# Kernel optimization log

Hardware: AMD Instinct MI355X
Metric: run time of the kernel (lower is better)

Reference implementation:

```python
import jax, jax.numpy as jnp
import numpy as np

N_NODES = 100000


def _add_self_loops(edge_index, n):
    loop = jnp.arange(n, dtype=edge_index.dtype)
    row = jnp.concatenate([edge_index[0], loop])
    col = jnp.concatenate([edge_index[1], loop])
    return row, col


def _gcn_conv(x, row, col, norm, W, b, n):
    # linear transform first (features shrink 512->16 before gather/scatter)
    h = x @ W                                  # [N, H]
    msg = h[row] * norm[:, None]               # [E+N, H] gather + scale
    out = jax.ops.segment_sum(msg, col, num_segments=n)  # scatter-add
    return out + b


def setup_inputs() -> dict:
    key = jax.random.key(0)
    ks = jax.random.split(key, 8)
    n, e, f, h = N_NODES, 3200000, 512, 16
    x = jax.random.normal(ks[0], (n, f), dtype=jnp.float32)
    edge_index = jax.random.randint(ks[1], (2, e), 0, n, dtype=jnp.int64)
    W1 = jax.random.normal(ks[2], (f, h), dtype=jnp.float32) / np.sqrt(f)
    b1 = jnp.zeros((h,), dtype=jnp.float32)
    W2 = jax.random.normal(ks[3], (h, h), dtype=jnp.float32) / np.sqrt(h)
    b2 = jnp.zeros((h,), dtype=jnp.float32)
    Wl = jax.random.normal(ks[4], (h, 1), dtype=jnp.float32) / np.sqrt(h)
    bl = jnp.zeros((1,), dtype=jnp.float32)
    return {"x": x, "edge_index": edge_index, "W1": W1, "b1": b1,
            "W2": W2, "b2": b2, "Wl": Wl, "bl": bl}


def reference(x, edge_index, W1, b1, W2, b2, Wl, bl):
    n = x.shape[0]
    row, col = _add_self_loops(edge_index, n)
    # symmetric GCN normalization: D^{-1/2} (A+I) D^{-1/2}
    deg = jax.ops.segment_sum(jnp.ones_like(col, dtype=x.dtype), col, num_segments=n)
    dinv = jnp.where(deg > 0, jax.lax.rsqrt(deg), 0.0)
    norm = dinv[row] * dinv[col]               # [E+N]

    out = jax.nn.relu(_gcn_conv(x, row, col, norm, W1, b1, n))
    out = jax.nn.relu(_gcn_conv(out, row, col, norm, W2, b2, n))
    return (out @ Wl + bl).reshape(-1)         # [N]
```

## Files before the change

kernel.cpp:

```cpp
#include <hip/hip_runtime.h>


#define NTHREADS 256

__global__ void hist_kernel(const int* __restrict__ col, int E, int n,
                            int* __restrict__ indeg) {
    int i = blockIdx.x * blockDim.x + threadIdx.x;
    int stride = gridDim.x * blockDim.x;
    for (; i < E; i += stride) {
        int c = col[i];
        if ((unsigned)c < (unsigned)n) atomicAdd(&indeg[c], 1);
    }
}

__global__ void dinv_kernel(const int* __restrict__ indeg,
                            float* __restrict__ dinv, int n) {
    int v = blockIdx.x * blockDim.x + threadIdx.x;
    if (v < n) dinv[v] = rsqrtf((float)(indeg[v] + 1));
}

__global__ void scan_block_sums(const int* __restrict__ indeg,
                                int* __restrict__ partial, int n) {
    __shared__ int s[NTHREADS];
    int t = threadIdx.x, i = blockIdx.x * NTHREADS + t;
    s[t] = (i < n) ? indeg[i] : 0;
    __syncthreads();
    for (int off = NTHREADS / 2; off > 0; off >>= 1) {
        if (t < off) s[t] += s[t + off];
        __syncthreads();
    }
    if (t == 0) partial[blockIdx.x] = s[0];
}

__global__ void scan_partials(int* __restrict__ partial, int nb,
                              int* __restrict__ rowptr, int n, int E) {
    __shared__ int s[512];
    int t = threadIdx.x;
    int v = (t < nb) ? partial[t] : 0;
    s[t] = v;
    __syncthreads();
    for (int off = 1; off < 512; off <<= 1) {
        int add = (t >= off) ? s[t - off] : 0;
        __syncthreads();
        s[t] += add;
        __syncthreads();
    }
    if (t < nb) partial[t] = s[t] - v;
    if (t == 0) rowptr[n] = E;
}

__global__ void scan_write(const int* __restrict__ indeg,
                           const int* __restrict__ partial,
                           int* __restrict__ rowptr, int n) {
    __shared__ int s[NTHREADS];
    int t = threadIdx.x, i = blockIdx.x * NTHREADS + t;
    int v = (i < n) ? indeg[i] : 0;
    s[t] = v;
    __syncthreads();
    for (int off = 1; off < NTHREADS; off <<= 1) {
        int add = (t >= off) ? s[t - off] : 0;
        __syncthreads();
        s[t] += add;
        __syncthreads();
    }
    if (i < n) rowptr[i] = partial[blockIdx.x] + s[t] - v;
}

__global__ void fill_kernel(const int* __restrict__ ei, int E, int n,
                            const int* __restrict__ rowptr,
                            int* __restrict__ cnt, int* __restrict__ adj) {
    int i = blockIdx.x * blockDim.x + threadIdx.x;
    int stride = gridDim.x * blockDim.x;
    for (; i < E; i += stride) {
        int r = ei[i];
        int c = ei[E + i];
        if ((unsigned)r >= (unsigned)n || (unsigned)c >= (unsigned)n) continue;
        int pos = rowptr[c] + atomicAdd(&cnt[c], 1);
        __builtin_nontemporal_store(r, &adj[pos]);
    }
}

__global__ void gemm1_kernel(const float* __restrict__ x,
                             const float* __restrict__ W1,
                             const float* __restrict__ dinv,
                             float* __restrict__ hs1, int n) {
    int v = blockIdx.x * blockDim.x + threadIdx.x;
    if (v >= n) return;
    const float4* xr = (const float4*)(x + (size_t)v * 512);
    float acc[16];
#pragma unroll
    for (int h = 0; h < 16; ++h) acc[h] = 0.f;
#pragma unroll 4
    for (int k4 = 0; k4 < 128; ++k4) {
        float4 xv = xr[k4];
        const float* wr = W1 + k4 * 64;
#pragma unroll
        for (int i = 0; i < 4; ++i) {
            float xs = (&xv.x)[i];
#pragma unroll
            for (int h = 0; h < 16; ++h)
                acc[h] = fmaf(xs, wr[i * 16 + h], acc[h]);
        }
    }
    float d = dinv[v];
    float4* o = (float4*)(hs1 + (size_t)v * 16);
#pragma unroll
    for (int q = 0; q < 4; ++q)
        o[q] = make_float4(acc[4 * q] * d, acc[4 * q + 1] * d,
                           acc[4 * q + 2] * d, acc[4 * q + 3] * d);
}

__global__ void agg1_kernel(const float* __restrict__ hs1,
                            const int* __restrict__ rowptr,
                            const int* __restrict__ adj,
                            const float* __restrict__ dinv,
                            const float* __restrict__ b1,
                            const float* __restrict__ W2,
                            float* __restrict__ hs2, int n) {
    __shared__ float w2s[256];
    int t = threadIdx.x;
    w2s[t] = W2[t];
    __syncthreads();
    int g = t >> 4, j = t & 15;
    int v = blockIdx.x * 16 + g;
    if (v >= n) return;
    int beg = rowptr[v], end = rowptr[v + 1];
    float acc = hs1[(size_t)v * 16 + j];
    float a0 = 0.f, a1 = 0.f, a2 = 0.f, a3 = 0.f;
    int i = beg;
    for (; i + 4 <= end; i += 4) {
        int u0 = adj[i], u1 = adj[i + 1], u2 = adj[i + 2], u3 = adj[i + 3];
        a0 += hs1[(size_t)u0 * 16 + j];
        a1 += hs1[(size_t)u1 * 16 + j];
        a2 += hs1[(size_t)u2 * 16 + j];
        a3 += hs1[(size_t)u3 * 16 + j];
    }
    for (; i < end; ++i) acc += hs1[(size_t)adj[i] * 16 + j];
    acc += (a0 + a1) + (a2 + a3);
    float d = dinv[v];
    float val = fmaxf(fmaf(d, acc, b1[j]), 0.f);
    float o = 0.f;
#pragma unroll
    for (int jj = 0; jj < 16; ++jj) {
        float bc = __shfl(val, (t & ~15) | jj);
        o = fmaf(bc, w2s[jj * 16 + j], o);
    }
    hs2[(size_t)v * 16 + j] = o * d;
}

__global__ void agg2_kernel(const float* __restrict__ hs2,
                            const int* __restrict__ rowptr,
                            const int* __restrict__ adj,
                            const float* __restrict__ dinv,
                            const float* __restrict__ b2,
                            const float* __restrict__ Wl,
                            const float* __restrict__ bl,
                            float* __restrict__ out, int n) {
    int t = threadIdx.x;
    int g = t >> 4, j = t & 15;
    int v = blockIdx.x * 16 + g;
    if (v >= n) return;
    int beg = rowptr[v], end = rowptr[v + 1];
    float acc = hs2[(size_t)v * 16 + j];
    float a0 = 0.f, a1 = 0.f, a2 = 0.f, a3 = 0.f;
    int i = beg;
    for (; i + 4 <= end; i += 4) {
        int u0 = adj[i], u1 = adj[i + 1], u2 = adj[i + 2], u3 = adj[i + 3];
        a0 += hs2[(size_t)u0 * 16 + j];
        a1 += hs2[(size_t)u1 * 16 + j];
        a2 += hs2[(size_t)u2 * 16 + j];
        a3 += hs2[(size_t)u3 * 16 + j];
    }
    for (; i < end; ++i) acc += hs2[(size_t)adj[i] * 16 + j];
    acc += (a0 + a1) + (a2 + a3);
    float d = dinv[v];
    float val = fmaxf(fmaf(d, acc, b2[j]), 0.f);
    float p = val * Wl[j];
#pragma unroll
    for (int off = 8; off > 0; off >>= 1)
        p += __shfl_down(p, off, 16);
    if (j == 0) out[v] = p + bl[0];
}

__global__ void scatter16_kernel(const float* __restrict__ src,
                                 float* __restrict__ dst,
                                 const int* __restrict__ ei,
                                 int E, int n) {
    int total = E * 16;
    int i = blockIdx.x * blockDim.x + threadIdx.x;
    int stride = gridDim.x * blockDim.x;
    for (; i < total; i += stride) {
        int e = i >> 4, j = i & 15;
        int u = ei[e];
        int v = ei[E + e];
        if ((unsigned)u < (unsigned)n && (unsigned)v < (unsigned)n)
            atomicAdd(&dst[(size_t)v * 16 + j], src[(size_t)u * 16 + j]);
    }
}

__global__ void xform1_kernel(float* __restrict__ hs2,
                              const float* __restrict__ dinv,
                              const float* __restrict__ b1,
                              const float* __restrict__ W2, int n) {
    __shared__ float w2s[256];
    int t = threadIdx.x;
    w2s[t] = W2[t];
    __syncthreads();
    int g = t >> 4, j = t & 15;
    int v = blockIdx.x * 16 + g;
    if (v >= n) return;
    float d = dinv[v];
    float val = fmaxf(fmaf(d, hs2[(size_t)v * 16 + j], b1[j]), 0.f);
    float o = 0.f;
#pragma unroll
    for (int jj = 0; jj < 16; ++jj) {
        float bc = __shfl(val, (t & ~15) | jj);
        o = fmaf(bc, w2s[jj * 16 + j], o);
    }
    hs2[(size_t)v * 16 + j] = o * d;
}

__global__ void xform2_kernel(const float* __restrict__ hs1,
                              const float* __restrict__ dinv,
                              const float* __restrict__ b2,
                              const float* __restrict__ Wl,
                              const float* __restrict__ bl,
                              float* __restrict__ out, int n) {
    int t = threadIdx.x;
    int g = t >> 4, j = t & 15;
    int v = blockIdx.x * 16 + g;
    if (v >= n) return;
    float d = dinv[v];
    float val = fmaxf(fmaf(d, hs1[(size_t)v * 16 + j], b2[j]), 0.f);
    float p = val * Wl[j];
#pragma unroll
    for (int off = 8; off > 0; off >>= 1)
        p += __shfl_down(p, off, 16);
    if (j == 0) out[v] = p + bl[0];
}

extern "C" void kernel_launch(void* const* d_in, const int* in_sizes, int n_in,
                              void* d_out, int out_size, void* d_ws, size_t ws_size,
                              hipStream_t stream) {
    const float* x  = (const float*)d_in[0];
    const int*   ei = (const int*)d_in[1];
    const float* W1 = (const float*)d_in[2];
    const float* b1 = (const float*)d_in[3];
    const float* W2 = (const float*)d_in[4];
    const float* b2 = (const float*)d_in[5];
    const float* Wl = (const float*)d_in[6];
    const float* bl = (const float*)d_in[7];
    float* out = (float*)d_out;

    const int n = in_sizes[0] / 512;
    const int E = in_sizes[1] / 2;

    char* ws = (char*)d_ws;
    size_t off = 0;
    auto alloc = [&](size_t bytes) {
        void* p = ws + off;
        off += (bytes + 255) & ~(size_t)255;
        return p;
    };

    const size_t sz_n4  = (size_t)n * 4;
    const size_t sz_hs  = (size_t)n * 16 * 4;
    const size_t REQ_CSR =
        4 * ((sz_n4 + 255 + 4) & ~(size_t)255) + 4096 +
        ((size_t)E * 4) + 2 * sz_hs + 4096;

    const int nb = (n + NTHREADS - 1) / NTHREADS;
    const int nodeblocks = (n + 15) / 16;

    if (ws_size == 0 || ws_size >= REQ_CSR) {
        int*   indeg   = (int*)alloc(sz_n4);
        int*   cnt     = (int*)alloc(sz_n4);
        float* dinv    = (float*)alloc(sz_n4);
        int*   rowptr  = (int*)alloc(sz_n4 + 4);
        int*   partial = (int*)alloc(4096);
        int*   adj     = (int*)alloc((size_t)E * 4);
        float* hs1     = (float*)alloc(sz_hs);
        float* hs2     = (float*)alloc(sz_hs);

        hipMemsetAsync(indeg, 0, sz_n4, stream);
        hipMemsetAsync(cnt, 0, sz_n4, stream);

        hist_kernel<<<4096, NTHREADS, 0, stream>>>(ei + E, E, n, indeg);
        dinv_kernel<<<nb, NTHREADS, 0, stream>>>(indeg, dinv, n);
        scan_block_sums<<<nb, NTHREADS, 0, stream>>>(indeg, partial, n);
        scan_partials<<<1, 512, 0, stream>>>(partial, nb, rowptr, n, E);
        scan_write<<<nb, NTHREADS, 0, stream>>>(indeg, partial, rowptr, n);
        fill_kernel<<<8192, NTHREADS, 0, stream>>>(ei, E, n, rowptr, cnt, adj);

        gemm1_kernel<<<nb, NTHREADS, 0, stream>>>(x, W1, dinv, hs1, n);
        agg1_kernel<<<nodeblocks, NTHREADS, 0, stream>>>(hs1, rowptr, adj, dinv,
                                                         b1, W2, hs2, n);
        agg2_kernel<<<nodeblocks, NTHREADS, 0, stream>>>(hs2, rowptr, adj, dinv,
                                                         b2, Wl, bl, out, n);
    } else {
        int*   indeg = (int*)alloc(sz_n4);
        float* dinv  = (float*)alloc(sz_n4);
        float* hs1   = (float*)alloc(sz_hs);
        float* hs2   = (float*)alloc(sz_hs);

        hipMemsetAsync(indeg, 0, sz_n4, stream);
        hist_kernel<<<4096, NTHREADS, 0, stream>>>(ei + E, E, n, indeg);
        dinv_kernel<<<nb, NTHREADS, 0, stream>>>(indeg, dinv, n);

        gemm1_kernel<<<nb, NTHREADS, 0, stream>>>(x, W1, dinv, hs1, n);

        hipMemcpyAsync(hs2, hs1, sz_hs, hipMemcpyDeviceToDevice, stream);
        scatter16_kernel<<<4096, NTHREADS, 0, stream>>>(hs1, hs2, ei, E, n);
        xform1_kernel<<<nodeblocks, NTHREADS, 0, stream>>>(hs2, dinv, b1, W2, n);

        hipMemcpyAsync(hs1, hs2, sz_hs, hipMemcpyDeviceToDevice, stream);
        scatter16_kernel<<<4096, NTHREADS, 0, stream>>>(hs2, hs1, ei, E, n);
        xform2_kernel<<<nodeblocks, NTHREADS, 0, stream>>>(hs1, dinv, b2, Wl,
                                                           bl, out, n);
    }
}
```

Before: 766.0 us.

## Build CSR via two-pass bucketed scatter to localize adjacency writes

Replaces the single random-scatter CSR fill with a two-pass binning: edges are first grouped into 128-node buckets (packed src<<7|local dst), then each bucket is scattered by one block into a small contiguous adj region. This aims to cut the cost of fully random 4-byte writes and atomics across the whole adjacency array. It adds an extra pass over E edges, an extra E*4 workspace buffer, and falls back to the old fill when workspace is small. hist_kernel now also checks source validity, and the fill grid size drops.

```diff
diff --git a/kernel.cpp b/kernel.cpp
--- a/kernel.cpp
+++ b/kernel.cpp
@@ -3,13 +3,15 @@
 
 #define NTHREADS 256
 
-__global__ void hist_kernel(const int* __restrict__ col, int E, int n,
+__global__ void hist_kernel(const int* __restrict__ ei, int E, int n,
                             int* __restrict__ indeg) {
     int i = blockIdx.x * blockDim.x + threadIdx.x;
     int stride = gridDim.x * blockDim.x;
     for (; i < E; i += stride) {
-        int c = col[i];
-        if ((unsigned)c < (unsigned)n) atomicAdd(&indeg[c], 1);
+        int r = ei[i];
+        int c = ei[E + i];
+        if ((unsigned)r < (unsigned)n && (unsigned)c < (unsigned)n)
+            atomicAdd(&indeg[c], 1);
     }
 }
 
@@ -76,7 +78,41 @@
         int c = ei[E + i];
         if ((unsigned)r >= (unsigned)n || (unsigned)c >= (unsigned)n) continue;
         int pos = rowptr[c] + atomicAdd(&cnt[c], 1);
-        __builtin_nontemporal_store(r, &adj[pos]);
+        adj[pos] = r;
+    }
+}
+
+__global__ void binfill_kernel(const int* __restrict__ ei, int E, int n,
+                               const int* __restrict__ rowptr,
+                               int* __restrict__ bfill,
+                               unsigned* __restrict__ bkt) {
+    int i = blockIdx.x * blockDim.x + threadIdx.x;
+    int stride = gridDim.x * blockDim.x;
+    for (; i < E; i += stride) {
+        int r = ei[i];
+        int c = ei[E + i];
+        if ((unsigned)r >= (unsigned)n || (unsigned)c >= (unsigned)n) continue;
+        int b = c >> 7;
+        int p = rowptr[b << 7] + atomicAdd(&bfill[b * 16], 1);
+        bkt[p] = ((unsigned)r << 7) | (unsigned)(c & 127);
+    }
+}
+
+__global__ void binscatter_kernel(const unsigned* __restrict__ bkt,
+                                  const int* __restrict__ rowptr,
+                                  int n, int* __restrict__ cnt,
+                                  int* __restrict__ adj) {
+    int b = blockIdx.x;
+    int base = b << 7;
+    int lo = rowptr[base];
+    int hiNode = base + 128; if (hiNode > n) hiNode = n;
+    int hi = rowptr[hiNode];
+    for (int idx = lo + threadIdx.x; idx < hi; idx += blockDim.x) {
+        unsigned e = bkt[idx];
+        int r = (int)(e >> 7);
+        int c = base | (int)(e & 127u);
+        int pos = rowptr[c] + atomicAdd(&cnt[c], 1);
+        adj[pos] = r;
     }
 }
 
@@ -254,6 +290,7 @@
 
     const int n = in_sizes[0] / 512;
     const int E = in_sizes[1] / 2;
+    const int NBKT = (n + 127) >> 7;
 
     char* ws = (char*)d_ws;
     size_t off = 0;
@@ -263,16 +300,20 @@
         return p;
     };
 
-    const size_t sz_n4  = (size_t)n * 4;
-    const size_t sz_hs  = (size_t)n * 16 * 4;
+    const size_t sz_n4 = (size_t)n * 4;
+    const size_t sz_hs = (size_t)n * 16 * 4;
     const size_t REQ_CSR =
         4 * ((sz_n4 + 255 + 4) & ~(size_t)255) + 4096 +
         ((size_t)E * 4) + 2 * sz_hs + 4096;
+    const size_t REQ_BIN = REQ_CSR + (size_t)E * 4 + (size_t)NBKT * 64 + 8192;
 
     const int nb = (n + NTHREADS - 1) / NTHREADS;
     const int nodeblocks = (n + 15) / 16;
 
-    if (ws_size == 0 || ws_size >= REQ_CSR) {
+    const bool has_bin = (ws_size >= REQ_BIN);
+    const bool has_csr = (ws_size == 0 || ws_size >= REQ_CSR);
+
+    if (has_csr) {
         int*   indeg   = (int*)alloc(sz_n4);
         int*   cnt     = (int*)alloc(sz_n4);
         float* dinv    = (float*)alloc(sz_n4);
@@ -285,12 +326,24 @@
         hipMemsetAsync(indeg, 0, sz_n4, stream);
         hipMemsetAsync(cnt, 0, sz_n4, stream);
 
-        hist_kernel<<<4096, NTHREADS, 0, stream>>>(ei + E, E, n, indeg);
+        hist_kernel<<<4096, NTHREADS, 0, stream>>>(ei, E, n, indeg);
         dinv_kernel<<<nb, NTHREADS, 0, stream>>>(indeg, dinv, n);
         scan_block_sums<<<nb, NTHREADS, 0, stream>>>(indeg, partial, n);
         scan_partials<<<1, 512, 0, stream>>>(partial, nb, rowptr, n, E);
         scan_write<<<nb, NTHREADS, 0, stream>>>(indeg, partial, rowptr, n);
-        fill_kernel<<<8192, NTHREADS, 0, stream>>>(ei, E, n, rowptr, cnt, adj);
+
+        if (has_bin) {
+            unsigned* bkt   = (unsigned*)alloc((size_t)E * 4);
+            int*      bfill = (int*)alloc((size_t)NBKT * 64);
+            hipMemsetAsync(bfill, 0, (size_t)NBKT * 64, stream);
+            binfill_kernel<<<2048, NTHREADS, 0, stream>>>(ei, E, n, rowptr,
+                                                          bfill, bkt);
+            binscatter_kernel<<<NBKT, NTHREADS, 0, stream>>>(bkt, rowptr, n,
+                                                             cnt, adj);
+        } else {
+            fill_kernel<<<2048, NTHREADS, 0, stream>>>(ei, E, n, rowptr, cnt,
+                                                       adj);
+        }
 
         gemm1_kernel<<<nb, NTHREADS, 0, stream>>>(x, W1, dinv, hs1, n);
         agg1_kernel<<<nodeblocks, NTHREADS, 0, stream>>>(hs1, rowptr, adj, dinv,
@@ -304,7 +357,7 @@
         float* hs2   = (float*)alloc(sz_hs);
 
         hipMemsetAsync(indeg, 0, sz_n4, stream);
-        hist_kernel<<<4096, NTHREADS, 0, stream>>>(ei + E, E, n, indeg);
+        hist_kernel<<<4096, NTHREADS, 0, stream>>>(ei, E, n, indeg);
         dinv_kernel<<<nb, NTHREADS, 0, stream>>>(indeg, dinv, n);
 
         gemm1_kernel<<<nb, NTHREADS, 0, stream>>>(x, W1, dinv, hs1, n);
```

New measurement: 799.3 us. 1.04x slower.
